# Kernel tuning notes

Hardware: AMD Instinct MI355X
Metric: run time of the kernel (lower is better)

The kernel has to match this reference:

```python
import jax, jax.numpy as jnp
import numpy as np

N_NODES = 50000
N_EDGES = 300000
F_IN = 11
D = 256


def _gcn_conv(h, src, dst, deg_inv_sqrt, W, b, n):
    """PyG GCNConv: out = D^{-1/2} (A + I) D^{-1/2} (h W) + b.
    src/dst already include self-loops; deg_inv_sqrt precomputed."""
    norm = deg_inv_sqrt[src] * deg_inv_sqrt[dst]          # [E+N]
    hw = h @ W                                            # [N, D]
    msg = hw[src] * norm[:, None]                         # [E+N, D]
    out = jax.ops.segment_sum(msg, dst, num_segments=n)   # [N, D]
    return out + b


def setup_inputs() -> dict:
    key = jax.random.key(0)
    ks = jax.random.split(key, 8)
    x = jax.random.normal(ks[0], (N_NODES, F_IN), dtype=jnp.float32)
    edge_index = jax.random.randint(ks[1], (2, N_EDGES), 0, N_NODES, dtype=jnp.int32)
    s = 0.05
    W_embed = jax.random.normal(ks[2], (F_IN, D), dtype=jnp.float32) * s
    b_embed = jnp.zeros((D,), dtype=jnp.float32)
    W1 = jax.random.normal(ks[3], (D, D), dtype=jnp.float32) * s
    b1 = jnp.zeros((D,), dtype=jnp.float32)
    W2 = jax.random.normal(ks[4], (D, D), dtype=jnp.float32) * s
    b2 = jnp.zeros((D,), dtype=jnp.float32)
    return {"x": x, "edge_index": edge_index, "W_embed": W_embed, "b_embed": b_embed,
            "W1": W1, "b1": b1, "W2": W2, "b2": b2}


def reference(x, edge_index, W_embed, b_embed, W1, b1, W2, b2):
    n = x.shape[0]
    # add self-loops (PyG GCNConv default add_self_loops=True)
    loop = jnp.arange(n, dtype=edge_index.dtype)
    src = jnp.concatenate([edge_index[0], loop])
    dst = jnp.concatenate([edge_index[1], loop])
    # symmetric normalization: deg over target index with unit edge weights
    deg = jax.ops.segment_sum(jnp.ones(src.shape, dtype=x.dtype), dst, num_segments=n)
    deg_inv_sqrt = jnp.where(deg > 0, jax.lax.rsqrt(jnp.maximum(deg, 1e-12)), 0.0)

    h = jax.nn.relu(x @ W_embed + b_embed)                # embed + relu
    h = jax.nn.relu(_gcn_conv(h, src, dst, deg_inv_sqrt, W1, b1, n))
    h = _gcn_conv(h, src, dst, deg_inv_sqrt, W2, b2, n)
    return h
```

## Files before the change

### kernel.cpp

```cpp
#include <hip/hip_runtime.h>

#define N_NODES 50000
#define N_EDGES 300000
#define N_TOT   350000
#define D       256
#define MPAD    50048
#define SCAN_B  196
#define GEMM_B  784

typedef __attribute__((ext_vector_type(8))) short bf16x8;
typedef __attribute__((ext_vector_type(4))) float f32x4;
typedef __attribute__((ext_vector_type(8))) unsigned short u16x8;
typedef __attribute__((ext_vector_type(4))) unsigned short u16x4;

__device__ __forceinline__ float bf2f(unsigned short b) {
    union { unsigned u; float f; } v; v.u = ((unsigned)b) << 16; return v.f;
}
__device__ __forceinline__ unsigned short f2bf(float f) {
    union { float f; unsigned u; } v; v.f = f;
    unsigned u = v.u;
    unsigned r = (u + 0x7FFFu + ((u >> 16) & 1u)) >> 16;
    return (unsigned short)r;
}
__device__ __forceinline__ void g2lds16(const unsigned short* g, unsigned short* l) {
    __builtin_amdgcn_global_load_lds(
        (const __attribute__((address_space(1))) void*)g,
        (__attribute__((address_space(3))) void*)l, 16, 0, 0);
}

__global__ __launch_bounds__(256) void k1_kernel(
        const float* __restrict__ x, const int* __restrict__ ei,
        const float* __restrict__ We, const float* __restrict__ be,
        const float* __restrict__ W1, const float* __restrict__ W2,
        int* __restrict__ cnt,
        unsigned short* __restrict__ Wt1, unsigned short* __restrict__ Wt2,
        unsigned short* __restrict__ hA) {
    int t = threadIdx.x, b = blockIdx.x;
    int tid = b * 256 + t;

    if (tid < N_TOT) {
        int dst = (tid < N_EDGES) ? ei[N_EDGES + tid] : (tid - N_EDGES);
        atomicAdd(&cnt[dst], 1);
    }
    if (tid < 2 * D * D) {
        int wsel = tid >> 16, rem = tid & 65535;
        int tt = rem >> 8, bb = rem & 255;
        const float* W = wsel ? W2 : W1;
        unsigned short* Wt = wsel ? Wt2 : Wt1;
        Wt[bb * D + tt] = f2bf(W[tt * D + bb]);
    }
    float w[11];
    #pragma unroll
    for (int k = 0; k < 11; ++k) w[k] = We[k * D + t];
    float bb = be[t];
    #pragma unroll
    for (int ni = 0; ni < 8; ++ni) {
        int node = b * 8 + ni;
        float acc = 0.f;
        if (node < N_NODES) {
            acc = bb;
            #pragma unroll
            for (int k = 0; k < 11; ++k) acc += x[node * 11 + k] * w[k];
            acc = fmaxf(acc, 0.f);
        }
        hA[(size_t)node * D + t] = f2bf(acc);
    }
}

__global__ __launch_bounds__(256) void k3_kernel(const int* __restrict__ ei,
                          const int* __restrict__ locs,
                          const int* __restrict__ bsum, const float* __restrict__ dis,
                          int* __restrict__ fc, int* __restrict__ rowptr,
                          int2* __restrict__ epk) {
    int tid = blockIdx.x * 256 + threadIdx.x;
    if (tid == 0) rowptr[0] = 0;
    if (tid < N_NODES)
        rowptr[tid + 1] = locs[tid] + bsum[tid >> 8];
    if (tid < N_TOT) {
        int src, dst;
        if (tid < N_EDGES) { src = ei[tid]; dst = ei[N_EDGES + tid]; }
        else               { src = dst = tid - N_EDGES; }
        int base = bsum[dst >> 8] + ((dst & 255) ? locs[dst - 1] : 0);
        int pos = base + atomicAdd(&fc[dst], 1);
        epk[pos] = make_int2(src, __float_as_int(dis[src] * dis[dst]));
    }
}

__global__ __launch_bounds__(256) void gemm_kernel(const unsigned short* __restrict__ A,
                                                   const unsigned short* __restrict__ Bt,
                                                   unsigned short* __restrict__ C,
                                                   const int* __restrict__ cnt,
                                                   float* __restrict__ dis,
                                                   int* __restrict__ locs,
                                                   int* __restrict__ bsum,
                                                   int* __restrict__ done) {
    __shared__ unsigned short lA[128 * 64];
    __shared__ unsigned short lB[128 * 64];
    __shared__ int ws[4];
    __shared__ int amLast;
    int t = threadIdx.x;
    int bid = blockIdx.x;

    int xcd = bid & 7, s = bid >> 3;
    int pair = xcd * 49 + (s >> 1);
    int ny   = s & 1;
    if (pair >= MPAD / 128) return;

    if (cnt && bid < SCAN_B) {
        int lane = t & 63, wv4 = t >> 6;
        int i = bid * 256 + t;
        int v = (i < N_NODES) ? cnt[i] : 0;
        if (i < N_NODES) dis[i] = rsqrtf((float)v);
        int ssum = v;
        #pragma unroll
        for (int d = 1; d < 64; d <<= 1) {
            int u = __shfl_up(ssum, d, 64);
            if (lane >= d) ssum += u;
        }
        if (lane == 63) ws[wv4] = ssum;
        __syncthreads();
        int off = 0;
        #pragma unroll
        for (int k = 0; k < 4; ++k) if (k < wv4) off += ws[k];
        ssum += off;
        if (i < N_NODES) locs[i] = ssum;
        if (t == 255) {
            bsum[bid] = ssum;
            __threadfence();
            amLast = (atomicAdd(done, 1) == SCAN_B - 1);
        }
        __syncthreads();
        if (amLast) {
            __threadfence();
            int vv = 0;
            if (t < SCAN_B)
                vv = __hip_atomic_load(&bsum[t], __ATOMIC_RELAXED, __HIP_MEMORY_SCOPE_AGENT);
        int ss = vv;
            #pragma unroll
            for (int d = 1; d < 64; d <<= 1) {
                int u = __shfl_up(ss, d, 64);
                if (lane >= d) ss += u;
            }
            __syncthreads();
            if (lane == 63) ws[wv4] = ss;
            __syncthreads();
            int off2 = 0;
            #pragma unroll
            for (int k = 0; k < 4; ++k) if (k < wv4) off2 += ws[k];
            ss += off2;
            if (t < SCAN_B) bsum[t] = ss - vv;
        }
        __syncthreads();
    }

    int wv = t >> 6, lane = t & 63;
    int m0 = pair * 128;
    int n0 = ny * 128;
    int moff = (wv & 1) * 64, noff = (wv >> 1) * 64;
    int q = lane >> 4, r = lane & 15;

    int srow[4], scol[4];
    #pragma unroll
    for (int j = 0; j < 4; ++j) {
        int idx = j * 256 + t;
        srow[j] = idx >> 3;
        scol[j] = ((idx & 7) ^ (srow[j] & 7)) * 8;
    }

    f32x4 acc[4][4] = {};
    for (int kk = 0; kk < D; kk += 64) {
        __syncthreads();
        #pragma unroll
        for (int j = 0; j < 4; ++j) {
            int idx = j * 256 + t;
            g2lds16(A  + (size_t)(m0 + srow[j]) * D + kk + scol[j], lA + idx * 8);
            g2lds16(Bt + (size_t)(n0 + srow[j]) * D + kk + scol[j], lB + idx * 8);
        }
        __syncthreads();
        #pragma unroll
        for (int ks = 0; ks < 2; ++ks) {
            bf16x8 a[4], b[4];
            #pragma unroll
            for (int mt = 0; mt < 4; ++mt) {
                int row = moff + mt * 16 + r;
                a[mt] = *(const bf16x8*)(lA + row * 64 + (((ks * 4 + q) ^ (r & 7)) * 8));
            }
            #pragma unroll
            for (int nt = 0; nt < 4; ++nt) {
                int row = noff + nt * 16 + r;
                b[nt] = *(const bf16x8*)(lB + row * 64 + (((ks * 4 + q) ^ (r & 7)) * 8));
            }
            #pragma unroll
            for (int mt = 0; mt < 4; ++mt)
                #pragma unroll
                for (int nt = 0; nt < 4; ++nt)
                    acc[mt][nt] = __builtin_amdgcn_mfma_f32_16x16x32_bf16(b[nt], a[mt], acc[mt][nt], 0, 0, 0);
        }
    }
    #pragma unroll
    for (int mt = 0; mt < 4; ++mt) {
        int mrow = m0 + moff + mt * 16 + r;
        #pragma unroll
        for (int nt = 0; nt < 4; ++nt) {
            int ncol = n0 + noff + nt * 16 + (q << 2);
            u16x4 o;
            #pragma unroll
            for (int i = 0; i < 4; ++i) o[i] = f2bf(acc[mt][nt][i]);
            *(u16x4*)(C + (size_t)mrow * D + ncol) = o;
        }
    }
}

__global__ __launch_bounds__(256) void agg_kernel(const unsigned short* __restrict__ hw,
                                                  const int* __restrict__ rowptr,
                                                  const int2* __restrict__ epk,
                                                  const float* __restrict__ bias,
                                                  unsigned short* __restrict__ out_bf,
                                                  float* __restrict__ out_f32,
                                                  int mode) {
    int wid  = threadIdx.x >> 6;
    int lane = threadIdx.x & 63;
    int node = blockIdx.x * 4 + wid;
    if (node >= N_NODES) return;
    int s0 = rowptr[node], s1 = rowptr[node + 1];
    int half = lane >> 5, hl = lane & 31;

    float acc[8] = {};
    for (int base = s0; base < s1; base += 64) {
        int ec = s1 - base; if (ec > 64) ec = 64;
        int srcl = 0; float nml = 0.f;
        if (lane < ec) {
            int2 ep = epk[base + lane];
            srcl = ep.x; nml = __int_as_float(ep.y);
        }
        int it = (ec + 1) >> 1;
        for (int i = 0; i < it; i += 4) {
            int   e0 = (2 * i + half) & 63;
            int   e1 = (2 * i + 2 + half) & 63;
            int   e2 = (2 * i + 4 + half) & 63;
            int   e3 = (2 * i + 6 + half) & 63;
            int   sa = __shfl(srcl, e0, 64);
            float na = __shfl(nml,  e0, 64);
            int   sb = __shfl(srcl, e1, 64);
            float nb = __shfl(nml,  e1, 64);
            int   sc = __shfl(srcl, e2, 64);
            float nc = __shfl(nml,  e2, 64);
            int   sd = __shfl(srcl, e3, 64);
            float nd = __shfl(nml,  e3, 64);
            u16x8 ha = *(const u16x8*)(hw + (size_t)sa * D + hl * 8);
            u16x8 hb = *(const u16x8*)(hw + (size_t)sb * D + hl * 8);
            u16x8 hc = *(const u16x8*)(hw + (size_t)sc * D + hl * 8);
            u16x8 hd = *(const u16x8*)(hw + (size_t)sd * D + hl * 8);
            #pragma unroll
            for (int k = 0; k < 8; ++k) acc[k] += na * bf2f(ha[k]);
            #pragma unroll
            for (int k = 0; k < 8; ++k) acc[k] += nb * bf2f(hb[k]);
            #pragma unroll
            for (int k = 0; k < 8; ++k) acc[k] += nc * bf2f(hc[k]);
            #pragma unroll
            for (int k = 0; k < 8; ++k) acc[k] += nd * bf2f(hd[k]);
        }
    }
    #pragma unroll
    for (int k = 0; k < 8; ++k) acc[k] += __shfl_xor(acc[k], 32, 64);

    if (lane < 32) {
        int c = hl * 8;
        float4 bv0 = *(const float4*)(bias + c);
        float4 bv1 = *(const float4*)(bias + c + 4);
        float v[8];
        v[0] = acc[0] + bv0.x; v[1] = acc[1] + bv0.y;
        v[2] = acc[2] + bv0.z; v[3] = acc[3] + bv0.w;
        v[4] = acc[4] + bv1.x; v[5] = acc[5] + bv1.y;
        v[6] = acc[6] + bv1.z; v[7] = acc[7] + bv1.w;
        if (mode) {
            u16x8 ov;
            #pragma unroll
            for (int k = 0; k < 8; ++k) ov[k] = f2bf(fmaxf(v[k], 0.f));
            *(u16x8*)(out_bf + (size_t)node * D + c) = ov;
        } else {
            float4 o0 = { v[0], v[1], v[2], v[3] };
            float4 o1 = { v[4], v[5], v[6], v[7] };
            *(float4*)(out_f32 + (size_t)node * D + c)     = o0;
            *(float4*)(out_f32 + (size_t)node * D + c + 4) = o1;
        }
    }
}

extern "C" void kernel_launch(void* const* d_in, const int* in_sizes, int n_in,
                              void* d_out, int out_size, void* d_ws, size_t ws_size,
                              hipStream_t stream) {
    const float* x  = (const float*)d_in[0];
    const int*   ei = (const int*)d_in[1];
    const float* We = (const float*)d_in[2];
    const float* be = (const float*)d_in[3];
    const float* W1 = (const float*)d_in[4];
    const float* b1 = (const float*)d_in[5];
    const float* W2 = (const float*)d_in[6];
    const float* b2 = (const float*)d_in[7];
    float* out = (float*)d_out;

    char* w = (char*)d_ws;
    auto alloc = [&](size_t bytes) {
        char* p = w;
        w += (bytes + 255) & ~(size_t)255;
        return p;
    };
    int*            cnt    = (int*)alloc((size_t)N_NODES * 4);
    int*            fc     = (int*)alloc((size_t)N_NODES * 4);
    int*            done   = (int*)alloc(4);
    size_t zero_span = (size_t)((char*)(done + 64) - (char*)cnt);
    int*            rowptr = (int*)alloc((size_t)(N_NODES + 1) * 4);
    int*            locs   = (int*)alloc((size_t)N_NODES * 4);
    int*            bsum   = (int*)alloc((size_t)SCAN_B * 4);
    float*          dis    = (float*)alloc((size_t)N_NODES * 4);
    int2*           epk    = (int2*)alloc((size_t)N_TOT * 8);
    unsigned short* Wt1    = (unsigned short*)alloc((size_t)D * D * 2);
    unsigned short* Wt2    = (unsigned short*)alloc((size_t)D * D * 2);
    unsigned short* hA     = (unsigned short*)alloc((size_t)MPAD * D * 2);
    unsigned short* hW     = (unsigned short*)alloc((size_t)MPAD * D * 2);

    hipMemsetAsync(cnt, 0, zero_span, stream);
    k1_kernel<<<MPAD / 8, 256, 0, stream>>>(x, ei, We, be, W1, W2, cnt, Wt1, Wt2, hA);

    gemm_kernel<<<GEMM_B, 256, 0, stream>>>(hA, Wt1, hW, cnt, dis, locs, bsum, done);
    k3_kernel<<<(N_TOT + 255) / 256, 256, 0, stream>>>(ei, locs, bsum, dis, fc,
                                                       rowptr, epk);
    agg_kernel<<<(N_NODES + 3) / 4, 256, 0, stream>>>(hW, rowptr, epk, b1,
                                                      hA, nullptr, 1);

    gemm_kernel<<<GEMM_B, 256, 0, stream>>>(hA, Wt2, hW, nullptr, nullptr, nullptr,
                                            nullptr, nullptr);
    agg_kernel<<<(N_NODES + 3) / 4, 256, 0, stream>>>(hW, rowptr, epk, b2,
                                                      nullptr, out, 0);
}
```

Baseline: 231.5 us.

## Reorder GCN layers to aggregate before GEMM and fuse embed into aggregation

Uses the associativity A·(hW) = (A·h)·W to aggregate before the matrix multiply in both layers. The first aggregation recomputes the 11-feature embed plus ReLU per edge from x, so no embedded node matrix is materialized. Bias, ReLU and the final fp32 store move into the GEMM epilogue, and the scan moves into its own kernel, out of the GEMM. The cost is recomputing the embed once per edge (11 FMAs times 4 channels per lane) and reading x rows as scattered gathers.

Result: slower. 264.7 us (+14.4%).

```diff
diff --git a/kernel.cpp b/kernel.cpp
--- a/kernel.cpp
+++ b/kernel.cpp
@@ -29,15 +29,11 @@
 }
 
 __global__ __launch_bounds__(256) void k1_kernel(
-        const float* __restrict__ x, const int* __restrict__ ei,
-        const float* __restrict__ We, const float* __restrict__ be,
+        const int* __restrict__ ei,
         const float* __restrict__ W1, const float* __restrict__ W2,
         int* __restrict__ cnt,
-        unsigned short* __restrict__ Wt1, unsigned short* __restrict__ Wt2,
-        unsigned short* __restrict__ hA) {
-    int t = threadIdx.x, b = blockIdx.x;
-    int tid = b * 256 + t;
-
+        unsigned short* __restrict__ Wt1, unsigned short* __restrict__ Wt2) {
+    int tid = blockIdx.x * 256 + threadIdx.x;
     if (tid < N_TOT) {
         int dst = (tid < N_EDGES) ? ei[N_EDGES + tid] : (tid - N_EDGES);
         atomicAdd(&cnt[dst], 1);
@@ -49,21 +45,58 @@
         unsigned short* Wt = wsel ? Wt2 : Wt1;
         Wt[bb * D + tt] = f2bf(W[tt * D + bb]);
     }
-    float w[11];
-    #pragma unroll
-    for (int k = 0; k < 11; ++k) w[k] = We[k * D + t];
-    float bb = be[t];
-    #pragma unroll
-    for (int ni = 0; ni < 8; ++ni) {
-        int node = b * 8 + ni;
-        float acc = 0.f;
-        if (node < N_NODES) {
-            acc = bb;
-            #pragma unroll
-            for (int k = 0; k < 11; ++k) acc += x[node * 11 + k] * w[k];
-            acc = fmaxf(acc, 0.f);
-        }
-        hA[(size_t)node * D + t] = f2bf(acc);
+}
+
+__global__ __launch_bounds__(256) void k2_kernel(const int* __restrict__ cnt,
+                                                 float* __restrict__ dis,
+                                                 int* __restrict__ locs,
+                                                 int* __restrict__ bsum,
+                                                 int* __restrict__ done) {
+    __shared__ int ws[4];
+    __shared__ int amLast;
+    int t = threadIdx.x;
+    int lane = t & 63, wv4 = t >> 6;
+    int i = blockIdx.x * 256 + t;
+    int v = (i < N_NODES) ? cnt[i] : 0;
+    if (i < N_NODES) dis[i] = rsqrtf((float)v);
+    int s = v;
+    #pragma unroll
+    for (int d = 1; d < 64; d <<= 1) {
+        int u = __shfl_up(s, d, 64);
+        if (lane >= d) s += u;
+    }
+    if (lane == 63) ws[wv4] = s;
+    __syncthreads();
+    int off = 0;
+    #pragma unroll
+    for (int k = 0; k < 4; ++k) if (k < wv4) off += ws[k];
+    s += off;
+    if (i < N_NODES) locs[i] = s;
+    if (t == 255) {
+        bsum[blockIdx.x] = s;
+        __threadfence();
+        amLast = (atomicAdd(done, 1) == SCAN_B - 1);
+    }
+    __syncthreads();
+    if (amLast) {
+        __threadfence();
+        int vv = 0;
+        if (t < SCAN_B)
+            vv = __hip_atomic_load(&bsum[t], __ATOMIC_RELAXED, __HIP_MEMORY_SCOPE_AGENT);
+        int ss = vv;
+        #pragma unroll
+        for (int d = 1; d < 64; d <<= 1) {
+            int u = __shfl_up(ss, d, 64);
+            if (lane >= d) ss += u;
+        }
+        __syncthreads();
+        if (lane == 63) ws[wv4] = ss;
+        __syncthreads();
+        int off2 = 0;
+        #pragma unroll
+        for (int k = 0; k < 4; ++k) if (k < wv4) off2 += ws[k];
+        ss += off2;
+        if (t < SCAN_B) bsum[t] = ss - vv;
     }
 }
 
@@ -86,138 +119,58 @@
     }
 }
 
-__global__ __launch_bounds__(256) void gemm_kernel(const unsigned short* __restrict__ A,
-                                                   const unsigned short* __restrict__ Bt,
-                                                   unsigned short* __restrict__ C,
-                                                   const int* __restrict__ cnt,
-                                                   float* __restrict__ dis,
-                                                   int* __restrict__ locs,
-                                                   int* __restrict__ bsum,
-                                                   int* __restrict__ done) {
-    __shared__ unsigned short lA[128 * 64];
-    __shared__ unsigned short lB[128 * 64];
-    __shared__ int ws[4];
-    __shared__ int amLast;
-    int t = threadIdx.x;
-    int bid = blockIdx.x;
-
-    int xcd = bid & 7, s = bid >> 3;
-    int pair = xcd * 49 + (s >> 1);
-    int ny   = s & 1;
-    if (pair >= MPAD / 128) return;
-
-    if (cnt && bid < SCAN_B) {
-        int lane = t & 63, wv4 = t >> 6;
-        int i = bid * 256 + t;
-        int v = (i < N_NODES) ? cnt[i] : 0;
-        if (i < N_NODES) dis[i] = rsqrtf((float)v);
-        int ssum = v;
-        #pragma unroll
-        for (int d = 1; d < 64; d <<= 1) {
-            int u = __shfl_up(ssum, d, 64);
-            if (lane >= d) ssum += u;
-        }
-        if (lane == 63) ws[wv4] = ssum;
-        __syncthreads();
-        int off = 0;
-        #pragma unroll
-        for (int k = 0; k < 4; ++k) if (k < wv4) off += ws[k];
-        ssum += off;
-        if (i < N_NODES) locs[i] = ssum;
-        if (t == 255) {
-            bsum[bid] = ssum;
-            __threadfence();
-            amLast = (atomicAdd(done, 1) == SCAN_B - 1);
-        }
-        __syncthreads();
-        if (amLast) {
-            __threadfence();
-            int vv = 0;
-            if (t < SCAN_B)
-                vv = __hip_atomic_load(&bsum[t], __ATOMIC_RELAXED, __HIP_MEMORY_SCOPE_AGENT);
-        int ss = vv;
-            #pragma unroll
-            for (int d = 1; d < 64; d <<= 1) {
-                int u = __shfl_up(ss, d, 64);
-                if (lane >= d) ss += u;
-            }
-            __syncthreads();
-            if (lane == 63) ws[wv4] = ss;
-            __syncthreads();
-            int off2 = 0;
-            #pragma unroll
-            for (int k = 0; k < 4; ++k) if (k < wv4) off2 += ws[k];
-            ss += off2;
-            if (t < SCAN_B) bsum[t] = ss - vv;
-        }
-        __syncthreads();
-    }
-
-    int wv = t >> 6, lane = t & 63;
-    int m0 = pair * 128;
-    int n0 = ny * 128;
-    int moff = (wv & 1) * 64, noff = (wv >> 1) * 64;
-    int q = lane >> 4, r = lane & 15;
-
-    int srow[4], scol[4];
-    #pragma unroll
-    for (int j = 0; j < 4; ++j) {
-        int idx = j * 256 + t;
-        srow[j] = idx >> 3;
-        scol[j] = ((idx & 7) ^ (srow[j] & 7)) * 8;
-    }
-
-    f32x4 acc[4][4] = {};
-    for (int kk = 0; kk < D; kk += 64) {
-        __syncthreads();
-        #pragma unroll
-        for (int j = 0; j < 4; ++j) {
-            int idx = j * 256 + t;
-            g2lds16(A  + (size_t)(m0 + srow[j]) * D + kk + scol[j], lA + idx * 8);
-            g2lds16(Bt + (size_t)(n0 + srow[j]) * D + kk + scol[j], lB + idx * 8);
-        }
-        __syncthreads();
-        #pragma unroll
-        for (int ks = 0; ks < 2; ++ks) {
-            bf16x8 a[4], b[4];
-            #pragma unroll
-            for (int mt = 0; mt < 4; ++mt) {
-                int row = moff + mt * 16 + r;
-                a[mt] = *(const bf16x8*)(lA + row * 64 + (((ks * 4 + q) ^ (r & 7)) * 8));
-            }
-            #pragma unroll
-            for (int nt = 0; nt < 4; ++nt) {
-                int row = noff + nt * 16 + r;
-                b[nt] = *(const bf16x8*)(lB + row * 64 + (((ks * 4 + q) ^ (r & 7)) * 8));
-            }
-            #pragma unroll
-            for (int mt = 0; mt < 4; ++mt)
+__global__ __launch_bounds__(256) void agg1r_kernel(
+        const float* __restrict__ x,
+        const float* __restrict__ We, const float* __restrict__ be,
+        const int* __restrict__ rowptr, const int2* __restrict__ epk,
+        unsigned short* __restrict__ g) {
+    int wid = threadIdx.x >> 6, lane = threadIdx.x & 63;
+    int node = blockIdx.x * 4 + wid;
+    if (node >= MPAD) return;
+    int d0 = lane * 4;
+    float w[11][4];
+    #pragma unroll
+    for (int k = 0; k < 11; ++k) {
+        float4 wv = *(const float4*)(We + k * D + d0);
+        w[k][0] = wv.x; w[k][1] = wv.y; w[k][2] = wv.z; w[k][3] = wv.w;
+    }
+    float4 bev = *(const float4*)(be + d0);
+    float acc[4] = {};
+    if (node < N_NODES) {
+        int s0 = rowptr[node], s1 = rowptr[node + 1];
+        for (int base = s0; base < s1; base += 64) {
+            int ec = s1 - base; if (ec > 64) ec = 64;
+            int srcl = 0; float nml = 0.f;
+            if (lane < ec) {
+                int2 ep = epk[base + lane];
+                srcl = ep.x; nml = __int_as_float(ep.y);
+            }
+            #pragma unroll 2
+            for (int e = 0; e < ec; ++e) {
+                int s = __builtin_amdgcn_readfirstlane(__shfl(srcl, e, 64));
+                float n = __shfl(nml, e, 64);
+                const float* xr = x + (size_t)s * 11;
+                float z0 = bev.x, z1 = bev.y, z2 = bev.z, z3 = bev.w;
                 #pragma unroll
-                for (int nt = 0; nt < 4; ++nt)
-                    acc[mt][nt] = __builtin_amdgcn_mfma_f32_16x16x32_bf16(b[nt], a[mt], acc[mt][nt], 0, 0, 0);
-        }
-    }
-    #pragma unroll
-    for (int mt = 0; mt < 4; ++mt) {
-        int mrow = m0 + moff + mt * 16 + r;
-        #pragma unroll
-        for (int nt = 0; nt < 4; ++nt) {
-            int ncol = n0 + noff + nt * 16 + (q << 2);
-            u16x4 o;
-            #pragma unroll
-            for (int i = 0; i < 4; ++i) o[i] = f2bf(acc[mt][nt][i]);
-            *(u16x4*)(C + (size_t)mrow * D + ncol) = o;
-        }
-    }
-}
-
-__global__ __launch_bounds__(256) void agg_kernel(const unsigned short* __restrict__ hw,
-                                                  const int* __restrict__ rowptr,
-                                                  const int2* __restrict__ epk,
-                                                  const float* __restrict__ bias,
-                                                  unsigned short* __restrict__ out_bf,
-                                                  float* __restrict__ out_f32,
-                                                  int mode) {
+                for (int k = 0; k < 11; ++k) {
+                    float xv = xr[k];
+                    z0 += xv * w[k][0]; z1 += xv * w[k][1];
+                    z2 += xv * w[k][2]; z3 += xv * w[k][3];
+                }
+                acc[0] += n * fmaxf(z0, 0.f); acc[1] += n * fmaxf(z1, 0.f);
+                acc[2] += n * fmaxf(z2, 0.f); acc[3] += n * fmaxf(z3, 0.f);
+            }
+        }
+    }
+    u16x4 o = { f2bf(acc[0]), f2bf(acc[1]), f2bf(acc[2]), f2bf(acc[3]) };
+    *(u16x4*)(g + (size_t)node * D + d0) = o;
+}
+
+__global__ __launch_bounds__(256) void agg2_kernel(
+        const unsigned short* __restrict__ hw,
+        const int* __restrict__ rowptr,
+        const int2* __restrict__ epk,
+        unsigned short* __restrict__ out_bf) {
     int wid  = threadIdx.x >> 6;
     int lane = threadIdx.x & 63;
     int node = blockIdx.x * 4 + wid;
@@ -266,23 +219,91 @@
 
     if (lane < 32) {
         int c = hl * 8;
-        float4 bv0 = *(const float4*)(bias + c);
-        float4 bv1 = *(const float4*)(bias + c + 4);
-        float v[8];
-        v[0] = acc[0] + bv0.x; v[1] = acc[1] + bv0.y;
-        v[2] = acc[2] + bv0.z; v[3] = acc[3] + bv0.w;
-        v[4] = acc[4] + bv1.x; v[5] = acc[5] + bv1.y;
-        v[6] = acc[6] + bv1.z; v[7] = acc[7] + bv1.w;
-        if (mode) {
-            u16x8 ov;
-            #pragma unroll
-            for (int k = 0; k < 8; ++k) ov[k] = f2bf(fmaxf(v[k], 0.f));
-            *(u16x8*)(out_bf + (size_t)node * D + c) = ov;
-        } else {
-            float4 o0 = { v[0], v[1], v[2], v[3] };
-            float4 o1 = { v[4], v[5], v[6], v[7] };
-            *(float4*)(out_f32 + (size_t)node * D + c)     = o0;
-            *(float4*)(out_f32 + (size_t)node * D + c + 4) = o1;
+        u16x8 ov;
+        #pragma unroll
+        for (int k = 0; k < 8; ++k) ov[k] = f2bf(acc[k]);
+        *(u16x8*)(out_bf + (size_t)node * D + c) = ov;
+    }
+}
+
+__global__ __launch_bounds__(256) void gemm_kernel(const unsigned short* __restrict__ A,
+                                                   const unsigned short* __restrict__ Bt,
+                                                   const float* __restrict__ bias,
+                                                   unsigned short* __restrict__ Cb,
+                                                   float* __restrict__ Cf,
+                                                   int mode) {
+    __shared__ unsigned short lA[128 * 64];
+    __shared__ unsigned short lB[128 * 64];
+    int t = threadIdx.x;
+    int bid = blockIdx.x;
+
+    int xcd = bid & 7, s = bid >> 3;
+    int pair = xcd * 49 + (s >> 1);
+    int ny   = s & 1;
+    if (pair >= MPAD / 128) return;
+
+    int wv = t >> 6, lane = t & 63;
+    int m0 = pair * 128;
+    int n0 = ny * 128;
+    int moff = (wv & 1) * 64, noff = (wv >> 1) * 64;
+    int q = lane >> 4, r = lane & 15;
+
+    int srow[4], scol[4];
+    #pragma unroll
+    for (int j = 0; j < 4; ++j) {
+        int idx = j * 256 + t;
+        srow[j] = idx >> 3;
+        scol[j] = ((idx & 7) ^ (srow[j] & 7)) * 8;
+    }
+
+    f32x4 acc[4][4] = {};
+    for (int kk = 0; kk < D; kk += 64) {
+        __syncthreads();
+        #pragma unroll
+        for (int j = 0; j < 4; ++j) {
+            int idx = j * 256 + t;
+            g2lds16(A  + (size_t)(m0 + srow[j]) * D + kk + scol[j], lA + idx * 8);
+            g2lds16(Bt + (size_t)(n0 + srow[j]) * D + kk + scol[j], lB + idx * 8);
+        }
+        __syncthreads();
+        #pragma unroll
+        for (int ks = 0; ks < 2; ++ks) {
+            bf16x8 a[4], b[4];
+            #pragma unroll
+            for (int mt = 0; mt < 4; ++mt) {
+                int row = moff + mt * 16 + r;
+                a[mt] = *(const bf16x8*)(lA + row * 64 + (((ks * 4 + q) ^ (r & 7)) * 8));
+            }
+            #pragma unroll
+            for (int nt = 0; nt < 4; ++nt) {
+                int row = noff + nt * 16 + r;
+                b[nt] = *(const bf16x8*)(lB + row * 64 + (((ks * 4 + q) ^ (r & 7)) * 8));
+            }
+            #pragma unroll
+            for (int mt = 0; mt < 4; ++mt)
+                #pragma unroll
+                for (int nt = 0; nt < 4; ++nt)
+                    acc[mt][nt] = __builtin_amdgcn_mfma_f32_16x16x32_bf16(b[nt], a[mt], acc[mt][nt], 0, 0, 0);
+        }
+    }
+    #pragma unroll
+    for (int mt = 0; mt < 4; ++mt) {
+        int mrow = m0 + moff + mt * 16 + r;
+        #pragma unroll
+        for (int nt = 0; nt < 4; ++nt) {
+            int ncol = n0 + noff + nt * 16 + (q << 2);
+            float4 bv = *(const float4*)(bias + ncol);
+            float v[4] = { acc[mt][nt][0] + bv.x, acc[mt][nt][1] + bv.y,
+                           acc[mt][nt][2] + bv.z, acc[mt][nt][3] + bv.w };
+            if (mode) {
+                u16x4 o;
+                #pragma unroll
+                for (int i = 0; i < 4; ++i) o[i] = f2bf(fmaxf(v[i], 0.f));
+                *(u16x4*)(Cb + (size_t)mrow * D + ncol) = o;
+            } else if (mrow < N_NODES) {
+                float4 o = { v[0], v[1], v[2], v[3] };
+                *(float4*)(Cf + (size_t)mrow * D + ncol) = o;
+            }
         }
     }
 }
@@ -317,20 +338,16 @@
     int2*           epk    = (int2*)alloc((size_t)N_TOT * 8);
     unsigned short* Wt1    = (unsigned short*)alloc((size_t)D * D * 2);
     unsigned short* Wt2    = (unsigned short*)alloc((size_t)D * D * 2);
-    unsigned short* hA     = (unsigned short*)alloc((size_t)MPAD * D * 2);
-    unsigned short* hW     = (unsigned short*)alloc((size_t)MPAD * D * 2);
+    unsigned short* g      = (unsigned short*)alloc((size_t)MPAD * D * 2);
+    unsigned short* h1     = (unsigned short*)alloc((size_t)MPAD * D * 2);
 
     hipMemsetAsync(cnt, 0, zero_span, stream);
-    k1_kernel<<<MPAD / 8, 256, 0, stream>>>(x, ei, We, be, W1, W2, cnt, Wt1, Wt2, hA);
-
-    gemm_kernel<<<GEMM_B, 256, 0, stream>>>(hA, Wt1, hW, cnt, dis, locs, bsum, done);
+    k1_kernel<<<(N_TOT + 255) / 256, 256, 0, stream>>>(ei, W1, W2, cnt, Wt1, Wt2);
+    k2_kernel<<<SCAN_B, 256, 0, stream>>>(cnt, dis, locs, bsum, done);
     k3_kernel<<<(N_TOT + 255) / 256, 256, 0, stream>>>(ei, locs, bsum, dis, fc,
                                                        rowptr, epk);
-    agg_kernel<<<(N_NODES + 3) / 4, 256, 0, stream>>>(hW, rowptr, epk, b1,
-                                                      hA, nullptr, 1);
-
-    gemm_kernel<<<GEMM_B, 256, 0, stream>>>(hA, Wt2, hW, nullptr, nullptr, nullptr,
-                                            nullptr, nullptr);
-    agg_kernel<<<(N_NODES + 3) / 4, 256, 0, stream>>>(hW, rowptr, epk, b2,
-                                                      nullptr, out, 0);
-}
+    agg1r_kernel<<<MPAD / 4, 256, 0, stream>>>(x, We, be, rowptr, epk, g);
+    gemm_kernel<<<GEMM_B, 256, 0, stream>>>(g, Wt1, b1, h1, nullptr, 1);
+    agg2_kernel<<<(N_NODES + 3) / 4, 256, 0, stream>>>(h1, rowptr, epk, g);
+    gemm_kernel<<<GEMM_B, 256, 0, stream>>>(g, Wt2, b2, nullptr, out, 0);
+}
```
